# Optimization experiments

Hardware: AMD Instinct MI355X
Metric: run time of the kernel (lower is better)

Reference implementation:

```python
import jax, jax.numpy as jnp
import numpy as np

N, IN_DIM, KEY_DIM, K, VAL_DIM = 100000, 512, 100, 8, 64


def setup_inputs() -> dict:
    key = jax.random.key(0)
    ks = jax.random.split(key, 7)
    s = 0.02
    return {
        "x": jax.random.normal(ks[0], (N, IN_DIM), dtype=jnp.float32),
        "Wk": jax.random.normal(ks[1], (KEY_DIM, IN_DIM), dtype=jnp.float32) * s,
        "bk": jax.random.normal(ks[2], (KEY_DIM,), dtype=jnp.float32) * s,
        "Wq": jax.random.normal(ks[3], (K, KEY_DIM), dtype=jnp.float32) * s,
        "bq": jax.random.normal(ks[4], (K,), dtype=jnp.float32) * s,
        "Wv": jax.random.normal(ks[5], (VAL_DIM, IN_DIM), dtype=jnp.float32) * s,
        "bv": jax.random.normal(ks[6], (VAL_DIM,), dtype=jnp.float32) * s,
    }


def reference(x, Wk, bk, Wq, bq, Wv, bv):
    # torch.nn.Linear: y = x @ W.T + b
    key = x @ Wk.T + bk                  # [N, key_dim]
    val = x @ Wv.T + bv                  # [N, val_dim]
    que = key @ Wq.T + bq                # [N, k]
    # att_norm == 'softmax': per-sample softmax over the k groups
    w = jax.nn.softmax(que, axis=-1)     # [N, k]
    # per-sample outer product w_i^T @ val_i -> [N, k, val_dim]
    x_group = w[:, :, None] * val[:, None, :]
    return x_group
```

## Files before the change

### kernel.cpp

```cpp
#include <hip/hip_runtime.h>

#define NROWS 100000
#define IN_DIM 512

typedef __attribute__((ext_vector_type(8))) short short8;
typedef __attribute__((ext_vector_type(4))) float f32x4;

__device__ inline unsigned short f2bf(float f) {
    union { float f; unsigned u; } v; v.f = f;
    unsigned u = v.u;
    return (unsigned short)((u + 0x7FFFu + ((u >> 16) & 1u)) >> 16);
}

__global__ void qg_prepack(const float* __restrict__ Wk, const float* __restrict__ bk,
                           const float* __restrict__ Wq, const float* __restrict__ bq,
                           const float* __restrict__ Wv,
                           unsigned short* __restrict__ Bp, float* __restrict__ qb) {
    int id = blockIdx.x * 256 + threadIdx.x;
    if (id < 8) {
        float s = bq[id];
        #pragma unroll 4
        for (int j = 0; j < 100; ++j) s += Wq[id * 100 + j] * bk[j];
        qb[id] = s;
    }
    if (id >= 5120) return;
    int lane = id & 63;
    int ks = (id >> 6) & 15;
    int t = id >> 10;
    int c = t * 16 + (lane & 15);
    int kk = ks * 32 + (lane >> 4) * 8;
    short8 pk;
    #pragma unroll
    for (int e = 0; e < 8; ++e) {
        int k2 = kk + e;
        float w;
        if (c < 64) {
            w = Wv[c * IN_DIM + k2];
        } else if (c < 72) {
            float s = 0.f;
            #pragma unroll 4
            for (int j = 0; j < 100; ++j) s += Wq[(c - 64) * 100 + j] * Wk[j * IN_DIM + k2];
            w = s;
        } else {
            w = 0.f;
        }
        pk[e] = (short)f2bf(w);
    }
    ((short8*)Bp)[id] = pk;
}

__global__ __launch_bounds__(128, 4) void qg_main(const float* __restrict__ x,
                                                  const float* __restrict__ bv,
                                                  const unsigned short* __restrict__ Bp,
                                                  const float* __restrict__ qb,
                                                  float* __restrict__ out) {
    __shared__ float vlds[2][16][68];
    __shared__ float wlds[2][16][8];
    const int tid = threadIdx.x;
    const int w = tid >> 6;
    const int lane = tid & 63;
    const int g = lane >> 4;
    const int cl = lane & 15;
    const int rowbase = blockIdx.x * 32 + w * 16;

    const float* ap = x + (size_t)(rowbase + cl) * IN_DIM + g * 8;
    const short8* bp8 = (const short8*)Bp + lane;

    f32x4 acc[5];
    #pragma unroll
    for (int t = 0; t < 5; ++t) acc[t] = (f32x4){0.f, 0.f, 0.f, 0.f};

    float4 A[3][2];
    short8 B[2][5];

    #pragma unroll
    for (int p = 0; p < 3; ++p) {
        A[p][0] = *(const float4*)(ap + p * 32);
        A[p][1] = *(const float4*)(ap + p * 32 + 4);
    }
    #pragma unroll
    for (int p = 0; p < 2; ++p)
        #pragma unroll
        for (int t = 0; t < 5; ++t)
            B[p][t] = bp8[(t * 16 + p) * 64];

    #pragma unroll
    for (int s = 0; s < 16; ++s) {
        const int ai = s % 3, bi = s % 2;
        float4 f0 = A[ai][0];
        float4 f1 = A[ai][1];
        short8 af;
        af[0] = (short)f2bf(f0.x); af[1] = (short)f2bf(f0.y);
        af[2] = (short)f2bf(f0.z); af[3] = (short)f2bf(f0.w);
        af[4] = (short)f2bf(f1.x); af[5] = (short)f2bf(f1.y);
        af[6] = (short)f2bf(f1.z); af[7] = (short)f2bf(f1.w);
        if (s + 3 < 16) {
            A[ai][0] = *(const float4*)(ap + (s + 3) * 32);
            A[ai][1] = *(const float4*)(ap + (s + 3) * 32 + 4);
        }
        #pragma unroll
        for (int t = 0; t < 5; ++t)
            acc[t] = __builtin_amdgcn_mfma_f32_16x16x32_bf16(af, B[bi][t], acc[t], 0, 0, 0);
        if (s + 2 < 16) {
            #pragma unroll
            for (int t = 0; t < 5; ++t)
                B[bi][t] = bp8[(t * 16 + s + 2) * 64];
        }
    }

    #pragma unroll
    for (int t = 0; t < 4; ++t) {
        float b = bv[t * 16 + cl];
        #pragma unroll
        for (int r = 0; r < 4; ++r)
            vlds[w][g * 4 + r][t * 16 + cl] = acc[t][r] + b;
    }
    if (cl < 8) {
        float b = qb[cl];
        #pragma unroll
        for (int r = 0; r < 4; ++r)
            wlds[w][g * 4 + r][cl] = acc[4][r] + b;
    }
    asm volatile("s_waitcnt lgkmcnt(0)" ::: "memory");

    if (lane < 16) {
        float q[8];
        float m = -1e30f;
        #pragma unroll
        for (int k = 0; k < 8; ++k) { q[k] = wlds[w][lane][k]; m = fmaxf(m, q[k]); }
        float ssum = 0.f;
        #pragma unroll
        for (int k = 0; k < 8; ++k) { q[k] = __expf(q[k] - m); ssum += q[k]; }
        float inv = 1.f / ssum;
        #pragma unroll
        for (int k = 0; k < 8; ++k) wlds[w][lane][k] = q[k] * inv;
    }
    asm volatile("s_waitcnt lgkmcnt(0)" ::: "memory");

    f32x4* outp = (f32x4*)out + (size_t)rowbase * 128;
    #pragma unroll
    for (int it = 0; it < 32; ++it) {
        int idx = it * 64 + lane;
        int row = idx >> 7;
        int j = idx & 127;
        float wgt = wlds[w][row][j >> 4];
        float4 vv = *(const float4*)&vlds[w][row][(j & 15) * 4];
        f32x4 o;
        o[0] = wgt * vv.x; o[1] = wgt * vv.y; o[2] = wgt * vv.z; o[3] = wgt * vv.w;
        __builtin_nontemporal_store(o, &outp[(size_t)row * 128 + j]);
    }
}

extern "C" void kernel_launch(void* const* d_in, const int* in_sizes, int n_in,
                              void* d_out, int out_size, void* d_ws, size_t ws_size,
                              hipStream_t stream) {
    const float* x  = (const float*)d_in[0];
    const float* Wk = (const float*)d_in[1];
    const float* bk = (const float*)d_in[2];
    const float* Wq = (const float*)d_in[3];
    const float* bq = (const float*)d_in[4];
    const float* Wv = (const float*)d_in[5];
    const float* bv = (const float*)d_in[6];
    float* out = (float*)d_out;

    unsigned short* Bp = (unsigned short*)d_ws;
    float* qb = (float*)((char*)d_ws + 81920);

    qg_prepack<<<20, 256, 0, stream>>>(Wk, bk, Wq, bq, Wv, Bp, qb);
    qg_main<<<3125, 128, 0, stream>>>(x, bv, Bp, qb, out);
}
```

Before: 107.1 us.

## Stream x tiles into LDS via async global_load_lds with swizzle

Switches the main kernel to one-wave blocks of 16 rows that issue all x loads for the tile at once as direct global-to-LDS transfers into a 32KB XOR-swizzled buffer. All B fragments are preloaded into registers, and each k-step waits on a decreasing vmcnt before reading its slice from LDS. The goal is to put the whole x tile in flight at once and hide HBM latency more fully than the old register triple-buffering did. In exchange, the block uses more LDS and many more registers (80 short8 B values), which limits occupancy. The vmcnt-based waiting also depends on the compiler issuing memory operations in the expected order.

Result: slower. 144.6 us (+35.1%).

```diff
diff --git a/kernel.cpp b/kernel.cpp
--- a/kernel.cpp
+++ b/kernel.cpp
@@ -5,6 +5,9 @@
 
 typedef __attribute__((ext_vector_type(8))) short short8;
 typedef __attribute__((ext_vector_type(4))) float f32x4;
+typedef unsigned int u32;
+typedef const __attribute__((address_space(1))) u32* gptr_t;
+typedef __attribute__((address_space(3))) u32* lptr_t;
 
 __device__ inline unsigned short f2bf(float f) {
     union { float f; unsigned u; } v; v.f = f;
@@ -49,77 +52,82 @@
     ((short8*)Bp)[id] = pk;
 }
 
-__global__ __launch_bounds__(128, 4) void qg_main(const float* __restrict__ x,
-                                                  const float* __restrict__ bv,
-                                                  const unsigned short* __restrict__ Bp,
-                                                  const float* __restrict__ qb,
-                                                  float* __restrict__ out) {
-    __shared__ float vlds[2][16][68];
-    __shared__ float wlds[2][16][8];
-    const int tid = threadIdx.x;
-    const int w = tid >> 6;
-    const int lane = tid & 63;
+__global__ __launch_bounds__(64, 1) void qg_main(const float* __restrict__ x,
+                                                 const float* __restrict__ bv,
+                                                 const unsigned short* __restrict__ Bp,
+                                                 const float* __restrict__ qb,
+                                                 float* __restrict__ out) {
+    __shared__ float xs[16 * 512];
+    __shared__ float vlds[16][68];
+    __shared__ float wlds[16][8];
+    const int lane = threadIdx.x;
     const int g = lane >> 4;
     const int cl = lane & 15;
-    const int rowbase = blockIdx.x * 32 + w * 16;
+    const int rowbase = blockIdx.x * 16;
 
-    const float* ap = x + (size_t)(rowbase + cl) * IN_DIM + g * 8;
     const short8* bp8 = (const short8*)Bp + lane;
+
+    short8 B[16][5];
+    #pragma unroll
+    for (int s = 0; s < 16; ++s)
+        #pragma unroll
+        for (int t = 0; t < 5; ++t)
+            B[s][t] = bp8[(t * 16 + s) * 64];
+
+    {
+        int o4a = lane, o4b = 64 + lane;
+        int rowa = o4a >> 3, cha = o4a & 7;
+        int rowb = o4b >> 3, chb = o4b & 7;
+        const float* srca = x + (size_t)(rowbase + rowa) * IN_DIM + (cha ^ (rowa & 7)) * 4;
+        const float* srcb = x + (size_t)(rowbase + rowb) * IN_DIM + (chb ^ (rowb & 7)) * 4;
+        #pragma unroll
+        for (int s = 0; s < 16; ++s) {
+            __builtin_amdgcn_global_load_lds((gptr_t)(const void*)(srca + s * 32),
+                (lptr_t)(void*)&xs[s * 512 + o4a * 4], 16, 0, 0);
+            __builtin_amdgcn_global_load_lds((gptr_t)(const void*)(srcb + s * 32),
+                (lptr_t)(void*)&xs[s * 512 + o4b * 4], 16, 0, 0);
+        }
+    }
 
     f32x4 acc[5];
     #pragma unroll
     for (int t = 0; t < 5; ++t) acc[t] = (f32x4){0.f, 0.f, 0.f, 0.f};
 
-    float4 A[3][2];
-    short8 B[2][5];
+    #define QSTEP(S, NW) do {                                                  \
+        asm volatile("s_waitcnt vmcnt(" #NW ")" ::: "memory");                 \
+        const float4* xs4_ = (const float4*)&xs[(S) * 512];                    \
+        float4 f0_ = xs4_[cl * 8 + ((g * 2) ^ (cl & 7))];                      \
+        float4 f1_ = xs4_[cl * 8 + ((g * 2 + 1) ^ (cl & 7))];                  \
+        short8 af_;                                                            \
+        af_[0] = (short)f2bf(f0_.x); af_[1] = (short)f2bf(f0_.y);              \
+        af_[2] = (short)f2bf(f0_.z); af_[3] = (short)f2bf(f0_.w);              \
+        af_[4] = (short)f2bf(f1_.x); af_[5] = (short)f2bf(f1_.y);              \
+        af_[6] = (short)f2bf(f1_.z); af_[7] = (short)f2bf(f1_.w);              \
+        acc[0] = __builtin_amdgcn_mfma_f32_16x16x32_bf16(af_, B[S][0], acc[0], 0, 0, 0); \
+        acc[1] = __builtin_amdgcn_mfma_f32_16x16x32_bf16(af_, B[S][1], acc[1], 0, 0, 0); \
+        acc[2] = __builtin_amdgcn_mfma_f32_16x16x32_bf16(af_, B[S][2], acc[2], 0, 0, 0); \
+        acc[3] = __builtin_amdgcn_mfma_f32_16x16x32_bf16(af_, B[S][3], acc[3], 0, 0, 0); \
+        acc[4] = __builtin_amdgcn_mfma_f32_16x16x32_bf16(af_, B[S][4], acc[4], 0, 0, 0); \
+    } while (0)
 
-    #pragma unroll
-    for (int p = 0; p < 3; ++p) {
-        A[p][0] = *(const float4*)(ap + p * 32);
-        A[p][1] = *(const float4*)(ap + p * 32 + 4);
-    }
-    #pragma unroll
-    for (int p = 0; p < 2; ++p)
-        #pragma unroll
-        for (int t = 0; t < 5; ++t)
-            B[p][t] = bp8[(t * 16 + p) * 64];
-
-    #pragma unroll
-    for (int s = 0; s < 16; ++s) {
-        const int ai = s % 3, bi = s % 2;
-        float4 f0 = A[ai][0];
-        float4 f1 = A[ai][1];
-        short8 af;
-        af[0] = (short)f2bf(f0.x); af[1] = (short)f2bf(f0.y);
-        af[2] = (short)f2bf(f0.z); af[3] = (short)f2bf(f0.w);
-        af[4] = (short)f2bf(f1.x); af[5] = (short)f2bf(f1.y);
-        af[6] = (short)f2bf(f1.z); af[7] = (short)f2bf(f1.w);
-        if (s + 3 < 16) {
-            A[ai][0] = *(const float4*)(ap + (s + 3) * 32);
-            A[ai][1] = *(const float4*)(ap + (s + 3) * 32 + 4);
-        }
-        #pragma unroll
-        for (int t = 0; t < 5; ++t)
-            acc[t] = __builtin_amdgcn_mfma_f32_16x16x32_bf16(af, B[bi][t], acc[t], 0, 0, 0);
-        if (s + 2 < 16) {
-            #pragma unroll
-            for (int t = 0; t < 5; ++t)
-                B[bi][t] = bp8[(t * 16 + s + 2) * 64];
-        }
-    }
+    QSTEP(0, 30);  QSTEP(1, 28);  QSTEP(2, 26);  QSTEP(3, 24);
+    QSTEP(4, 22);  QSTEP(5, 20);  QSTEP(6, 18);  QSTEP(7, 16);
+    QSTEP(8, 14);  QSTEP(9, 12);  QSTEP(10, 10); QSTEP(11, 8);
+    QSTEP(12, 6);  QSTEP(13, 4);  QSTEP(14, 2);  QSTEP(15, 0);
+    #undef QSTEP
 
     #pragma unroll
     for (int t = 0; t < 4; ++t) {
         float b = bv[t * 16 + cl];
         #pragma unroll
         for (int r = 0; r < 4; ++r)
-            vlds[w][g * 4 + r][t * 16 + cl] = acc[t][r] + b;
+            vlds[g * 4 + r][t * 16 + cl] = acc[t][r] + b;
     }
     if (cl < 8) {
         float b = qb[cl];
         #pragma unroll
         for (int r = 0; r < 4; ++r)
-            wlds[w][g * 4 + r][cl] = acc[4][r] + b;
+            wlds[g * 4 + r][cl] = acc[4][r] + b;
     }
     asm volatile("s_waitcnt lgkmcnt(0)" ::: "memory");
 
@@ -127,13 +135,13 @@
         float q[8];
         float m = -1e30f;
         #pragma unroll
-        for (int k = 0; k < 8; ++k) { q[k] = wlds[w][lane][k]; m = fmaxf(m, q[k]); }
+        for (int k = 0; k < 8; ++k) { q[k] = wlds[lane][k]; m = fmaxf(m, q[k]); }
         float ssum = 0.f;
         #pragma unroll
         for (int k = 0; k < 8; ++k) { q[k] = __expf(q[k] - m); ssum += q[k]; }
         float inv = 1.f / ssum;
         #pragma unroll
-        for (int k = 0; k < 8; ++k) wlds[w][lane][k] = q[k] * inv;
+        for (int k = 0; k < 8; ++k) wlds[lane][k] = q[k] * inv;
     }
     asm volatile("s_waitcnt lgkmcnt(0)" ::: "memory");
 
@@ -143,8 +151,8 @@
         int idx = it * 64 + lane;
         int row = idx >> 7;
         int j = idx & 127;
-        float wgt = wlds[w][row][j >> 4];
-        float4 vv = *(const float4*)&vlds[w][row][(j & 15) * 4];
+        float wgt = wlds[row][j >> 4];
+        float4 vv = *(const float4*)&vlds[row][(j & 15) * 4];
         f32x4 o;
         o[0] = wgt * vv.x; o[1] = wgt * vv.y; o[2] = wgt * vv.z; o[3] = wgt * vv.w;
         __builtin_nontemporal_store(o, &outp[(size_t)row * 128 + j]);
@@ -167,5 +175,5 @@
     float* qb = (float*)((char*)d_ws + 81920);
 
     qg_prepack<<<20, 256, 0, stream>>>(Wk, bk, Wq, bq, Wv, Bp, qb);
-    qg_main<<<3125, 128, 0, stream>>>(x, bv, Bp, qb, out);
+    qg_main<<<6250, 64, 0, stream>>>(x, bv, Bp, qb, out);
 }
```

## Split fused kernel into GEMM pass and separate outer-product expansion pass

Applied to the files above, without the earlier changes.

The single fused kernel becomes two. The first kernel runs the bf16 MFMA projection and softmax, then stores each row's value vector and softmax weights into the tail of that row's output as scratch. A second kernel reads that scratch into shared memory and writes the full k-by-val_dim outer product with nontemporal stores. The aim is to separate the compute-bound GEMM from the store-heavy expansion so each can be scheduled on its own, at the cost of an extra launch and an extra global write and read of the scratch data.

Result: slower. 126.5 us (+18.2%).

```diff
diff --git a/kernel.cpp b/kernel.cpp
--- a/kernel.cpp
+++ b/kernel.cpp
@@ -49,7 +49,7 @@
     ((short8*)Bp)[id] = pk;
 }
 
-__global__ __launch_bounds__(128, 4) void qg_main(const float* __restrict__ x,
+__global__ __launch_bounds__(128, 4) void qg_gemm(const float* __restrict__ x,
                                                   const float* __restrict__ bv,
                                                   const unsigned short* __restrict__ Bp,
                                                   const float* __restrict__ qb,
@@ -72,7 +72,6 @@
 
     float4 A[3][2];
     short8 B[2][5];
-
     #pragma unroll
     for (int p = 0; p < 3; ++p) {
         A[p][0] = *(const float4*)(ap + p * 32);
@@ -137,17 +136,63 @@
     }
     asm volatile("s_waitcnt lgkmcnt(0)" ::: "memory");
 
+    #pragma unroll
+    for (int it = 0; it < 4; ++it) {
+        int idx = it * 64 + lane;
+        int row = idx >> 4;
+        int v4 = idx & 15;
+        float4 vv = *(const float4*)&vlds[w][row][v4 * 4];
+        *(float4*)(out + (size_t)(rowbase + row) * 512 + 448 + v4 * 4) = vv;
+    }
+    #pragma unroll
+    for (int it = 0; it < 2; ++it) {
+        int idx = it * 64 + lane;
+        int row = idx >> 3;
+        int kk = idx & 7;
+        out[(size_t)(rowbase + row) * 512 + 440 + kk] = wlds[w][row][kk];
+    }
+}
+
+__global__ __launch_bounds__(256) void qg_expand(float* __restrict__ out) {
+    __shared__ float vlds[4][16][68];
+    __shared__ float wlds[4][16][8];
+    const int tid = threadIdx.x;
+    const int w = tid >> 6;
+    const int lane = tid & 63;
+    const int rowbase = blockIdx.x * 64 + w * 16;
+
+    #pragma unroll
+    for (int it = 0; it < 4; ++it) {
+        int idx = it * 64 + lane;
+        int row = idx >> 4;
+        int v4 = idx & 15;
+        int gr = min(rowbase + row, NROWS - 1);
+        float4 vv = *(const float4*)(out + (size_t)gr * 512 + 448 + v4 * 4);
+        *(float4*)&vlds[w][row][v4 * 4] = vv;
+    }
+    #pragma unroll
+    for (int it = 0; it < 2; ++it) {
+        int idx = it * 64 + lane;
+        int row = idx >> 3;
+        int kk = idx & 7;
+        int gr = min(rowbase + row, NROWS - 1);
+        wlds[w][row][kk] = out[(size_t)gr * 512 + 440 + kk];
+    }
+    asm volatile("s_waitcnt vmcnt(0) lgkmcnt(0)" ::: "memory");
+
     f32x4* outp = (f32x4*)out + (size_t)rowbase * 128;
     #pragma unroll
     for (int it = 0; it < 32; ++it) {
         int idx = it * 64 + lane;
         int row = idx >> 7;
         int j = idx & 127;
-        float wgt = wlds[w][row][j >> 4];
-        float4 vv = *(const float4*)&vlds[w][row][(j & 15) * 4];
-        f32x4 o;
-        o[0] = wgt * vv.x; o[1] = wgt * vv.y; o[2] = wgt * vv.z; o[3] = wgt * vv.w;
-        __builtin_nontemporal_store(o, &outp[(size_t)row * 128 + j]);
+        if (rowbase + row < NROWS) {
+            float wgt = wlds[w][row][j >> 4];
+            float4 vv = *(const float4*)&vlds[w][row][(j & 15) * 4];
+            f32x4 o;
+            o[0] = wgt * vv.x; o[1] = wgt * vv.y; o[2] = wgt * vv.z; o[3] = wgt * vv.w;
+            __builtin_nontemporal_store(o, &outp[(size_t)row * 128 + j]);
+        }
     }
 }
 
@@ -167,5 +212,6 @@
     float* qb = (float*)((char*)d_ws + 81920);
 
     qg_prepack<<<20, 256, 0, stream>>>(Wk, bk, Wq, bq, Wv, Bp, qb);
-    qg_main<<<3125, 128, 0, stream>>>(x, bv, Bp, qb, out);
-}
+    qg_gemm<<<3125, 128, 0, stream>>>(x, bv, Bp, qb, out);
+    qg_expand<<<1563, 256, 0, stream>>>(out);
+}
```

## Process 32 rows per wave to reuse B fragments across two MFMA tiles

Applied to the files above, without the earlier changes.

Each wave now handles two 16-row M tiles, sharing each loaded weight fragment across both tiles' MFMAs and halving the grid. The x prefetch depth drops to two stages while the B prefetch grows to three, and a sched_barrier separates loads from MFMAs. Row indices are clamped and stores guarded because the row count no longer divides evenly. This raises register and LDS use per block and lowers the launch-bounds occupancy hint, which may hurt latency hiding in a bandwidth-bound kernel.

Result: faster. 104.4 us (-2.5%).

```diff
diff --git a/kernel.cpp b/kernel.cpp
--- a/kernel.cpp
+++ b/kernel.cpp
@@ -49,81 +49,94 @@
     ((short8*)Bp)[id] = pk;
 }
 
-__global__ __launch_bounds__(128, 4) void qg_main(const float* __restrict__ x,
+__global__ __launch_bounds__(128, 2) void qg_main(const float* __restrict__ x,
                                                   const float* __restrict__ bv,
                                                   const unsigned short* __restrict__ Bp,
                                                   const float* __restrict__ qb,
                                                   float* __restrict__ out) {
-    __shared__ float vlds[2][16][68];
-    __shared__ float wlds[2][16][8];
+    __shared__ float vlds[2][32][68];
+    __shared__ float wlds[2][32][8];
     const int tid = threadIdx.x;
     const int w = tid >> 6;
     const int lane = tid & 63;
     const int g = lane >> 4;
     const int cl = lane & 15;
-    const int rowbase = blockIdx.x * 32 + w * 16;
+    const int rowbase = (blockIdx.x * 2 + w) * 32;
 
-    const float* ap = x + (size_t)(rowbase + cl) * IN_DIM + g * 8;
+    const float* ap0 = x + (size_t)min(rowbase + cl,      NROWS - 1) * IN_DIM + g * 8;
+    const float* ap1 = x + (size_t)min(rowbase + 16 + cl, NROWS - 1) * IN_DIM + g * 8;
     const short8* bp8 = (const short8*)Bp + lane;
 
-    f32x4 acc[5];
+    f32x4 acc[2][5];
     #pragma unroll
-    for (int t = 0; t < 5; ++t) acc[t] = (f32x4){0.f, 0.f, 0.f, 0.f};
+    for (int m = 0; m < 2; ++m)
+        #pragma unroll
+        for (int t = 0; t < 5; ++t) acc[m][t] = (f32x4){0.f, 0.f, 0.f, 0.f};
 
-    float4 A[3][2];
-    short8 B[2][5];
+    float4 A[2][2][2];
+    short8 B[3][5];
 
     #pragma unroll
-    for (int p = 0; p < 3; ++p) {
-        A[p][0] = *(const float4*)(ap + p * 32);
-        A[p][1] = *(const float4*)(ap + p * 32 + 4);
+    for (int p = 0; p < 2; ++p) {
+        A[p][0][0] = *(const float4*)(ap0 + p * 32);
+        A[p][0][1] = *(const float4*)(ap0 + p * 32 + 4);
+        A[p][1][0] = *(const float4*)(ap1 + p * 32);
+        A[p][1][1] = *(const float4*)(ap1 + p * 32 + 4);
+        #pragma unroll
+        for (int t = 0; t < 5; ++t) B[p][t] = bp8[(t * 16 + p) * 64];
     }
-    #pragma unroll
-    for (int p = 0; p < 2; ++p)
-        #pragma unroll
-        for (int t = 0; t < 5; ++t)
-            B[p][t] = bp8[(t * 16 + p) * 64];
 
     #pragma unroll
     for (int s = 0; s < 16; ++s) {
-        const int ai = s % 3, bi = s % 2;
-        float4 f0 = A[ai][0];
-        float4 f1 = A[ai][1];
-        short8 af;
-        af[0] = (short)f2bf(f0.x); af[1] = (short)f2bf(f0.y);
-        af[2] = (short)f2bf(f0.z); af[3] = (short)f2bf(f0.w);
-        af[4] = (short)f2bf(f1.x); af[5] = (short)f2bf(f1.y);
-        af[6] = (short)f2bf(f1.z); af[7] = (short)f2bf(f1.w);
-        if (s + 3 < 16) {
-            A[ai][0] = *(const float4*)(ap + (s + 3) * 32);
-            A[ai][1] = *(const float4*)(ap + (s + 3) * 32 + 4);
+        const int ai = s & 1, bi = s % 3;
+        short8 af[2];
+        #pragma unroll
+        for (int m = 0; m < 2; ++m) {
+            float4 f0 = A[ai][m][0];
+            float4 f1 = A[ai][m][1];
+            af[m][0] = (short)f2bf(f0.x); af[m][1] = (short)f2bf(f0.y);
+            af[m][2] = (short)f2bf(f0.z); af[m][3] = (short)f2bf(f0.w);
+            af[m][4] = (short)f2bf(f1.x); af[m][5] = (short)f2bf(f1.y);
+            af[m][6] = (short)f2bf(f1.z); af[m][7] = (short)f2bf(f1.w);
         }
+        if (s + 2 < 16) {
+            A[ai][0][0] = *(const float4*)(ap0 + (s + 2) * 32);
+            A[ai][0][1] = *(const float4*)(ap0 + (s + 2) * 32 + 4);
+            A[ai][1][0] = *(const float4*)(ap1 + (s + 2) * 32);
+            A[ai][1][1] = *(const float4*)(ap1 + (s + 2) * 32 + 4);
+            #pragma unroll
+            for (int t = 0; t < 5; ++t)
+                B[(s + 2) % 3][t] = bp8[(t * 16 + s + 2) * 64];
+        }
+        __builtin_amdgcn_sched_barrier(0);
         #pragma unroll
         for (int t = 0; t < 5; ++t)
-            acc[t] = __builtin_amdgcn_mfma_f32_16x16x32_bf16(af, B[bi][t], acc[t], 0, 0, 0);
-        if (s + 2 < 16) {
-            #pragma unroll
-            for (int t = 0; t < 5; ++t)
-                B[bi][t] = bp8[(t * 16 + s + 2) * 64];
-        }
+            acc[0][t] = __builtin_amdgcn_mfma_f32_16x16x32_bf16(af[0], B[bi][t], acc[0][t], 0, 0, 0);
+        #pragma unroll
+        for (int t = 0; t < 5; ++t)
+            acc[1][t] = __builtin_amdgcn_mfma_f32_16x16x32_bf16(af[1], B[bi][t], acc[1][t], 0, 0, 0);
     }
 
     #pragma unroll
     for (int t = 0; t < 4; ++t) {
         float b = bv[t * 16 + cl];
         #pragma unroll
-        for (int r = 0; r < 4; ++r)
-            vlds[w][g * 4 + r][t * 16 + cl] = acc[t][r] + b;
+        for (int m = 0; m < 2; ++m)
+            #pragma unroll
+            for (int r = 0; r < 4; ++r)
+                vlds[w][m * 16 + g * 4 + r][t * 16 + cl] = acc[m][t][r] + b;
     }
     if (cl < 8) {
         float b = qb[cl];
         #pragma unroll
-        for (int r = 0; r < 4; ++r)
-            wlds[w][g * 4 + r][cl] = acc[4][r] + b;
+        for (int m = 0; m < 2; ++m)
+            #pragma unroll
+            for (int r = 0; r < 4; ++r)
+                wlds[w][m * 16 + g * 4 + r][cl] = acc[m][4][r] + b;
     }
     asm volatile("s_waitcnt lgkmcnt(0)" ::: "memory");
 
-    if (lane < 16) {
+    if (lane < 32) {
         float q[8];
         float m = -1e30f;
         #pragma unroll
@@ -139,15 +152,17 @@
 
     f32x4* outp = (f32x4*)out + (size_t)rowbase * 128;
     #pragma unroll
-    for (int it = 0; it < 32; ++it) {
+    for (int it = 0; it < 64; ++it) {
         int idx = it * 64 + lane;
         int row = idx >> 7;
         int j = idx & 127;
-        float wgt = wlds[w][row][j >> 4];
-        float4 vv = *(const float4*)&vlds[w][row][(j & 15) * 4];
-        f32x4 o;
-        o[0] = wgt * vv.x; o[1] = wgt * vv.y; o[2] = wgt * vv.z; o[3] = wgt * vv.w;
-        __builtin_nontemporal_store(o, &outp[(size_t)row * 128 + j]);
+        if (rowbase + row < NROWS) {
+            float wgt = wlds[w][row][j >> 4];
+            float4 vv = *(const float4*)&vlds[w][row][(j & 15) * 4];
+            f32x4 o;
+            o[0] = wgt * vv.x; o[1] = wgt * vv.y; o[2] = wgt * vv.z; o[3] = wgt * vv.w;
+            __builtin_nontemporal_store(o, &outp[(size_t)row * 128 + j]);
+        }
     }
 }
 
@@ -167,5 +182,5 @@
     float* qb = (float*)((char*)d_ws + 81920);
 
     qg_prepack<<<20, 256, 0, stream>>>(Wk, bk, Wq, bq, Wv, Bp, qb);
-    qg_main<<<3125, 128, 0, stream>>>(x, bv, Bp, qb, out);
+    qg_main<<<1563, 128, 0, stream>>>(x, bv, Bp, qb, out);
 }
```
